# Kernel optimization log

Measured on AMD Instinct MI355X. Metric: run time of the kernel, lower is better.

Reference implementation:

```python
import jax, jax.numpy as jnp
import numpy as np

EPS = 1e-6
K = 20
B, N = 4, 4096
HID, CDIM = 128, 64


def vn_lin(W, x):
    # W: [Cout, Cin], x: [B, Cin, 3, ...] -> [B, Cout, 3, ...]
    return jnp.einsum('oc,bc...->bo...', W, x)


def vn_leaky(x, d, ns=0.0):
    # vector-neuron leaky ReLU: reflect the part of x anti-aligned with direction d
    dot = jnp.sum(x * d, axis=2, keepdims=True)
    dsq = jnp.sum(d * d, axis=2, keepdims=True)
    return ns * x + (1.0 - ns) * jnp.where(dot >= 0, x, x - (dot / (dsq + EPS)) * d)


def vn_max_pool(x, Wd):
    # pool over the LAST axis, picking per-(b,c) the vector maximizing <x, d>
    d = vn_lin(Wd, x)
    dot = jnp.sum(x * d, axis=2, keepdims=True)            # [B,C,1,...,L]
    idx = jnp.broadcast_to(jnp.argmax(dot, axis=-1), x.shape[:-1])
    return jnp.take_along_axis(x, idx[..., None], axis=-1)[..., 0]


def graph_feature_cross(pts, k):
    # pts: [B, N, 3] -> [B, 3ch, 3vec, N, k] with channels (nbr-x, x, cross(nbr,x))
    sq = jnp.sum(pts * pts, axis=-1)
    inner = jnp.einsum('bnd,bmd->bnm', pts, pts)
    neg_dist = 2.0 * inner - sq[:, :, None] - sq[:, None, :]
    _, idx = jax.lax.top_k(neg_dist, k)                     # [B, N, k]
    nbr = jax.vmap(lambda p, i: p[i])(pts, idx)             # [B, N, k, 3]
    x = jnp.broadcast_to(pts[:, :, None, :], nbr.shape)
    cross = jnp.cross(nbr, x, axis=-1)
    feat = jnp.stack([nbr - x, x, cross], axis=3)           # [B, N, k, 3ch, 3vec]
    return jnp.transpose(feat, (0, 3, 4, 1, 2))


def resblock(x, a0, f0, a1, f1, sc):
    net = vn_lin(f0, vn_leaky(x, vn_lin(a0, x)))
    dx = vn_lin(f1, vn_leaky(net, vn_lin(a1, net)))
    return vn_lin(sc, x) + dx


def _init(key, shape, fan_in):
    return jax.random.normal(key, shape, jnp.float32) / np.sqrt(fan_in)


def setup_inputs():
    key = jax.random.key(0)
    ks = jax.random.split(key, 14)
    return {
        'pc': jax.random.normal(ks[0], (B, N, 3), jnp.float32),
        'conv_Wf': _init(ks[1], (64, 3), 3),
        'conv_Wd': _init(ks[2], (64, 3), 3),
        'pool_pos_Wd': _init(ks[3], (64, 64), 64),
        'fc_pos_W': _init(ks[4], (2 * HID, 64), 64),
        'blk_a0': _init(ks[5], (5, 2 * HID, 2 * HID), 2 * HID),
        'blk_f0': _init(ks[6], (5, HID, 2 * HID), 2 * HID),
        'blk_a1': _init(ks[7], (5, HID, HID), HID),
        'blk_f1': _init(ks[8], (5, HID, HID), HID),
        'blk_sc': _init(ks[9], (5, HID, 2 * HID), 2 * HID),
        'pool_Wd': _init(ks[10], (5, HID, HID), HID),
        'actc_Wd': _init(ks[11], (HID, HID), HID),
        'fcc_W': _init(ks[12], (CDIM, HID), HID),
    }


def reference(pc, conv_Wf, conv_Wd, pool_pos_Wd, fc_pos_W, blk_a0, blk_f0, blk_a1, blk_f1, blk_sc, pool_Wd, actc_Wd, fcc_W):
    b = pc.shape[0]
    feat = graph_feature_cross(pc, K)                         # [B,3,3,N,k]
    net = vn_leaky(vn_lin(conv_Wf, feat), vn_lin(conv_Wd, feat))  # [B,64,3,N,k]
    net = vn_max_pool(net, pool_pos_Wd)                       # [B,64,3,N] (pool over k)
    net = vn_lin(fc_pos_W, net)                               # [B,256,3,N]
    for i in range(5):
        net = resblock(net, blk_a0[i], blk_f0[i], blk_a1[i], blk_f1[i], blk_sc[i])  # [B,128,3,N]
        if i < 4:
            pooled = vn_max_pool(net, pool_Wd[i])             # [B,128,3] (pool over N)
            net = jnp.concatenate([net, jnp.broadcast_to(pooled[..., None], net.shape)], axis=1)
    net = vn_max_pool(net, pool_Wd[4])                        # [B,128,3]
    c = vn_lin(fcc_W, vn_leaky(net, vn_lin(actc_Wd, net)))    # [B,64,3]
    return c.reshape(b, -1)                                   # [B,192]
```

## Files before the change

### kernel.cpp

```cpp
#include <hip/hip_runtime.h>
#include <hip/hip_bf16.h>
#include <math.h>

#define NPTS 4096
#define NB 4
#define KNN 20
#define NCOLS (3*NPTS)
#define NEG_INF (-__builtin_huge_valf())
#define DNEG_INF (-__builtin_huge_val())

typedef _Float16 f16x8 __attribute__((ext_vector_type(8)));
typedef float f32x4 __attribute__((ext_vector_type(4)));

#define WOFF_FC 0
#define WOFF_A0 16384
#define WOFF_F0 344064
#define WOFF_A1 507904
#define WOFF_F1 589824
#define WOFF_SC 671744
#define WOFF_PW 835584
#define WTOT    917504

__global__ __launch_bounds__(512) void knn_kernel(const float* __restrict__ pc,
                                                  int* __restrict__ idx) {
  __shared__ float pts[NPTS*3];
  __shared__ double msv[2][8];
  __shared__ int    msn[2][8];
  int b = blockIdx.x >> 10;
  int rowblk = blockIdx.x & 1023;
  const float* pb = pc + (size_t)b*NPTS*3;
  for (int i = threadIdx.x; i < NPTS*3; i += 512) pts[i] = pb[i];
  __syncthreads();
  int wave = threadIdx.x >> 6;
  int lane = threadIdx.x & 63;
  int row  = wave >> 1;
  int half = wave & 1;
  int l128 = half*64 + lane;
  int n = rowblk*4 + row;
  double pn0 = pts[n*3+0], pn1 = pts[n*3+1], pn2 = pts[n*3+2];
  double sqn = pn0*pn0 + pn1*pn1 + pn2*pn2;
  double nd[32];
#pragma unroll
  for (int j = 0; j < 32; ++j) {
    int m = j*128 + l128;
    double q0 = pts[m*3+0], q1 = pts[m*3+1], q2 = pts[m*3+2];
    double inner = pn0*q0 + pn1*q1 + pn2*q2;
    double sqm = q0*q0 + q1*q1 + q2*q2;
    nd[j] = 2.0*inner - sqn - sqm;
  }
  double gm[2]; int gj[2];
#pragma unroll
  for (int g = 0; g < 2; ++g) {
    double v = nd[g*16]; int jb = g*16;
#pragma unroll
    for (int jj = 1; jj < 16; ++jj) {
      int j = g*16 + jj;
      bool take = nd[j] > v;
      v = take ? nd[j] : v;
      jb = take ? j : jb;
    }
    gm[g] = v; gj[g] = jb;
  }
  int* orow = idx + ((size_t)b*NPTS + n)*KNN;
  for (int t = 0; t < KNN; ++t) {
    double bv = gm[0]; int bj = gj[0];
    if (gm[1] > bv) { bv = gm[1]; bj = gj[1]; }
    int bm = bj*128 + l128;
#pragma unroll
    for (int s = 1; s < 64; s <<= 1) {
      double ov = __shfl_xor(bv, s, 64);
      int om = __shfl_xor(bm, s, 64);
      bool take = (ov > bv) || (ov == bv && om < bm);
      bv = take ? ov : bv;
      bm = take ? om : bm;
    }
    if (lane == 0) { msv[t&1][wave] = bv; msn[t&1][wave] = bm; }
    __syncthreads();
    {
      double pv = msv[t&1][wave^1]; int pm = msn[t&1][wave^1];
      bool take = (pv > bv) || (pv == bv && pm < bm);
      bv = take ? pv : bv;
      bm = take ? pm : bm;
    }
    if (half == 0 && lane == 0) orow[t] = bm;
    if (t < KNN-1) {
      int vic_l128 = bm & 127;
      int jw = bm >> 7;
      int vic_half = vic_l128 >> 6;
      if (vic_half == half) {
        bool iswl = (l128 == vic_l128);
        int gw = jw >> 4;
#define REBUILD(G) { \
  _Pragma("unroll") \
  for (int jj = 0; jj < 16; ++jj) { \
    int j = (G)*16 + jj; \
    if (iswl && j == jw) nd[j] = DNEG_INF; \
  } \
  double v = nd[(G)*16]; int jb = (G)*16; \
  _Pragma("unroll") \
  for (int jj = 1; jj < 16; ++jj) { \
    int j = (G)*16 + jj; \
    bool take = nd[j] > v; \
    v = take ? nd[j] : v; \
    jb = take ? j : jb; \
  } \
  gm[G] = v; gj[G] = jb; \
}
        if (gw == 0) REBUILD(0)
        else         REBUILD(1)
#undef REBUILD
      }
    }
  }
}

#define ECH 5
__global__ __launch_bounds__(128) void edgeconv_kernel(
    const float* __restrict__ pc, const int* __restrict__ knnidx,
    const float* __restrict__ Wf, const float* __restrict__ Wd,
    const float* __restrict__ Wp, float* __restrict__ outp) {
  __shared__ float xls[2*ECH*3*64];
  int wave = threadIdx.x >> 6, lane = threadIdx.x & 63;
  int pid0 = blockIdx.x * 2;
  int b = pid0 >> 12;
  int n = (pid0 & (NPTS-1)) + wave;
  const float* pb = pc + (size_t)b*NPTS*3;
  int c = lane;
  float wrow[64];
#pragma unroll
  for (int j = 0; j < 64; ++j) wrow[j] = Wp[c*64 + j];
  float wf0 = Wf[c*3+0], wf1 = Wf[c*3+1], wf2 = Wf[c*3+2];
  float wd0 = Wd[c*3+0], wd1 = Wd[c*3+1], wd2 = Wd[c*3+2];
  float f9[9];
#pragma unroll
  for (int i = 0; i < 9; ++i) f9[i] = 0.0f;
  if (lane < KNN) {
    int j = knnidx[((size_t)b*NPTS + n)*KNN + lane];
    float q0 = pb[j*3+0], q1 = pb[j*3+1], q2 = pb[j*3+2];
    float x0 = pb[n*3+0], x1 = pb[n*3+1], x2 = pb[n*3+2];
    f9[0] = q0-x0; f9[1] = q1-x1; f9[2] = q2-x2;
    f9[3] = x0;    f9[4] = x1;    f9[5] = x2;
    f9[6] = q1*x2 - q2*x1;
    f9[7] = q2*x0 - q0*x2;
    f9[8] = q0*x1 - q1*x0;
  }
  float* xw = &xls[wave*ECH*3*64];
  double bdot = DNEG_INF;
  float bx0 = 0.f, bx1 = 0.f, bx2 = 0.f;
  for (int k0 = 0; k0 < KNN; k0 += ECH) {
    for (int kc = 0; kc < ECH; ++kc) {
      int kk = k0 + kc;
      float fch[9];
#pragma unroll
      for (int i = 0; i < 9; ++i) fch[i] = __shfl(f9[i], kk, 64);
      float fv[3], dv[3];
#pragma unroll
      for (int v = 0; v < 3; ++v) {
        fv[v] = wf0*fch[v] + wf1*fch[3+v] + wf2*fch[6+v];
        dv[v] = wd0*fch[v] + wd1*fch[3+v] + wd2*fch[6+v];
      }
      float dot = fv[0]*dv[0] + fv[1]*dv[1] + fv[2]*dv[2];
      if (dot < 0.0f) {
        float dsq = dv[0]*dv[0] + dv[1]*dv[1] + dv[2]*dv[2];
        float s = dot / (dsq + 1e-6f);
        fv[0] -= s*dv[0]; fv[1] -= s*dv[1]; fv[2] -= s*dv[2];
      }
      xw[(0*ECH+kc)*64 + c] = fv[0];
      xw[(1*ECH+kc)*64 + c] = fv[1];
      xw[(2*ECH+kc)*64 + c] = fv[2];
    }
    for (int kc = 0; kc < ECH; ++kc) {
      float a0 = 0.f, a1 = 0.f, a2 = 0.f;
#pragma unroll
      for (int j = 0; j < 64; j += 4) {
        float4 v0 = *(const float4*)&xw[(0*ECH+kc)*64 + j];
        float4 v1 = *(const float4*)&xw[(1*ECH+kc)*64 + j];
        float4 v2 = *(const float4*)&xw[(2*ECH+kc)*64 + j];
        a0 += wrow[j]*v0.x + wrow[j+1]*v0.y + wrow[j+2]*v0.z + wrow[j+3]*v0.w;
        a1 += wrow[j]*v1.x + wrow[j+1]*v1.y + wrow[j+2]*v1.z + wrow[j+3]*v1.w;
        a2 += wrow[j]*v2.x + wrow[j+1]*v2.y + wrow[j+2]*v2.z + wrow[j+3]*v2.w;
      }
      float xc0 = xw[(0*ECH+kc)*64 + c];
      float xc1 = xw[(1*ECH+kc)*64 + c];
      float xc2 = xw[(2*ECH+kc)*64 + c];
      double dd = (double)xc0*a0 + (double)xc1*a1 + (double)xc2*a2;
      bool take = dd > bdot;
      bdot = take ? dd : bdot;
      bx0 = take ? xc0 : bx0;
      bx1 = take ? xc1 : bx1;
      bx2 = take ? xc2 : bx2;
    }
  }
  outp[((size_t)b*NCOLS + 0*NPTS + n)*64 + c] = bx0;
  outp[((size_t)b*NCOLS + 1*NPTS + n)*64 + c] = bx1;
  outp[((size_t)b*NCOLS + 2*NPTS + n)*64 + c] = bx2;
}

__global__ __launch_bounds__(256) void wsplit_kernel(
    const float* __restrict__ fc, const float* __restrict__ a0,
    const float* __restrict__ f0, const float* __restrict__ a1,
    const float* __restrict__ f1, const float* __restrict__ sc,
    const float* __restrict__ pw, _Float16* __restrict__ outp) {
  int i = blockIdx.x*256 + threadIdx.x;
  const float* src; int off;
  if      (i < WOFF_A0) { src = fc; off = WOFF_FC; }
  else if (i < WOFF_F0) { src = a0; off = WOFF_A0; }
  else if (i < WOFF_A1) { src = f0; off = WOFF_F0; }
  else if (i < WOFF_F1) { src = a1; off = WOFF_A1; }
  else if (i < WOFF_SC) { src = f1; off = WOFF_F1; }
  else if (i < WOFF_PW) { src = sc; off = WOFF_SC; }
  else                  { src = pw; off = WOFF_PW; }
  float w = src[i - off];
  _Float16 h = (_Float16)w;
  outp[i] = h;
  outp[i + WTOT] = (_Float16)(w - (float)h);
}

__global__ __launch_bounds__(256) void bias_kernel(
    const float* __restrict__ W, const float* __restrict__ pooled,
    float* __restrict__ bias, int Cout, int Wstride) {
  int id = blockIdx.x*256 + threadIdx.x;
  int co = id % Cout; int t = id / Cout;
  int v = t % 3; int b = t / 3;
  double acc = 0.0;
  const float* wr = W + (size_t)co*Wstride + 128;
  const float* pp = pooled + (size_t)b*384 + v;
#pragma unroll 4
  for (int c = 0; c < 128; ++c)
    acc += (double)wr[c] * (double)pp[c*3];
  bias[id] = (float)acc;
}

#define LDP 40
__global__ __launch_bounds__(256) void gemm_mfma(
    const _Float16* __restrict__ Wh, const _Float16* __restrict__ Wl,
    const float* __restrict__ X, const float* __restrict__ Z,
    const float* __restrict__ bias, float* __restrict__ Y,
    int Cin, int Wstride, int ldX, int ldY, int ldZ, int addZ, int Cbias) {
  __shared__ __align__(16) _Float16 Ah[64*LDP];
  __shared__ __align__(16) _Float16 Al[64*LDP];
  __shared__ __align__(16) _Float16 Bh[128*LDP];
  __shared__ __align__(16) _Float16 Bl[128*LDP];
  int b = blockIdx.z;
  int sp0 = blockIdx.x * 64;
  int co0 = blockIdx.y * 128;
  const float* Xb = X + ((size_t)b*NCOLS + sp0) * ldX;
  int t = threadIdx.x;
  int arow = t >> 2, akoff = (t & 3) * 8;
  int brow = t >> 1, bkoff = (t & 1) * 16;
  int wid = t >> 6, lane = t & 63;
  int wr = (wid >> 1) * 32, wc = (wid & 1) * 64;
  int lrow = lane & 15, lk = (lane >> 4) * 8;
  f32x4 acc[2][4];
#pragma unroll
  for (int f = 0; f < 2; ++f)
#pragma unroll
    for (int g = 0; g < 4; ++g)
#pragma unroll
      for (int r = 0; r < 4; ++r) acc[f][g][r] = 0.0f;

  for (int k0 = 0; k0 < Cin; k0 += 32) {
    const float* xs = Xb + (size_t)arow*ldX + k0 + akoff;
    float xv[8];
    *(float4*)&xv[0] = *(const float4*)&xs[0];
    *(float4*)&xv[4] = *(const float4*)&xs[4];
    _Float16 xh[8], xl[8];
#pragma unroll
    for (int j = 0; j < 8; ++j) {
      _Float16 h = (_Float16)xv[j];
      xh[j] = h; xl[j] = (_Float16)(xv[j] - (float)h);
    }
    *(f16x8*)&Ah[arow*LDP + akoff] = *(f16x8*)&xh[0];
    *(f16x8*)&Al[arow*LDP + akoff] = *(f16x8*)&xl[0];
    const _Float16* whs = Wh + (size_t)(co0 + brow)*Wstride + k0 + bkoff;
    const _Float16* wls = Wl + (size_t)(co0 + brow)*Wstride + k0 + bkoff;
    *(f16x8*)&Bh[brow*LDP + bkoff]     = *(const f16x8*)&whs[0];
    *(f16x8*)&Bh[brow*LDP + bkoff + 8] = *(const f16x8*)&whs[8];
    *(f16x8*)&Bl[brow*LDP + bkoff]     = *(const f16x8*)&wls[0];
    *(f16x8*)&Bl[brow*LDP + bkoff + 8] = *(const f16x8*)&wls[8];
    __syncthreads();
    f16x8 ah[2], al[2], bh[4], bl[4];
#pragma unroll
    for (int f = 0; f < 2; ++f) {
      ah[f] = *(f16x8*)&Ah[(wr + f*16 + lrow)*LDP + lk];
      al[f] = *(f16x8*)&Al[(wr + f*16 + lrow)*LDP + lk];
    }
#pragma unroll
    for (int g = 0; g < 4; ++g) {
      bh[g] = *(f16x8*)&Bh[(wc + g*16 + lrow)*LDP + lk];
      bl[g] = *(f16x8*)&Bl[(wc + g*16 + lrow)*LDP + lk];
    }
#pragma unroll
    for (int f = 0; f < 2; ++f)
#pragma unroll
      for (int g = 0; g < 4; ++g) {
        acc[f][g] = __builtin_amdgcn_mfma_f32_16x16x32_f16(ah[f], bh[g], acc[f][g], 0, 0, 0);
        acc[f][g] = __builtin_amdgcn_mfma_f32_16x16x32_f16(ah[f], bl[g], acc[f][g], 0, 0, 0);
        acc[f][g] = __builtin_amdgcn_mfma_f32_16x16x32_f16(al[f], bh[g], acc[f][g], 0, 0, 0);
      }
    __syncthreads();
  }
  int lr0 = (lane >> 4) * 4, lc = lane & 15;
  float badd[4] = {0.f, 0.f, 0.f, 0.f};
  if (bias) {
    int v = sp0 >> 12;
    const float* brow2 = bias + ((size_t)b*3 + v)*Cbias;
#pragma unroll
    for (int g = 0; g < 4; ++g) badd[g] = brow2[co0 + wc + g*16 + lc];
  }
#pragma unroll
  for (int f = 0; f < 2; ++f)
#pragma unroll
    for (int g = 0; g < 4; ++g)
#pragma unroll
      for (int r = 0; r < 4; ++r) {
        int sp = sp0 + wr + f*16 + lr0 + r;
        int co = co0 + wc + g*16 + lc;
        float val = acc[f][g][r] + badd[g];
        if (addZ) val += Z[((size_t)b*NCOLS + sp)*ldZ + co];
        Y[((size_t)b*NCOLS + sp)*ldY + co] = val;
      }
}

__global__ __launch_bounds__(256) void leaky_kernel(
    const float* __restrict__ X, float* __restrict__ D,
    const float* __restrict__ pooled,
    int cmask, int cshift, int ld) {
  long id = (long)blockIdx.x*256 + threadIdx.x;
  int c = (int)(id & cmask);
  long r = id >> cshift;
  int n = (int)(r & (NPTS-1));
  int b = (int)(r >> 12);
  size_t base = ((size_t)b*NCOLS + n)*ld + c;
  size_t vs = (size_t)NPTS*ld;
  float x0, x1, x2;
  if (pooled != nullptr && c >= 128) {
    const float* pp = pooled + (size_t)b*384 + (c - 128)*3;
    x0 = pp[0]; x1 = pp[1]; x2 = pp[2];
  } else {
    x0 = X[base]; x1 = X[base+vs]; x2 = X[base+2*vs];
  }
  float d0 = D[base], d1 = D[base+vs], d2 = D[base+2*vs];
  float dot = x0*d0 + x1*d1 + x2*d2;
  float u0 = x0, u1 = x1, u2 = x2;
  if (dot < 0.0f) {
    float dsq = d0*d0 + d1*d1 + d2*d2;
    float s = dot / (dsq + 1e-6f);
    u0 = x0 - s*d0; u1 = x1 - s*d1; u2 = x2 - s*d2;
  }
  D[base] = u0; D[base+vs] = u1; D[base+2*vs] = u2;
}

__global__ __launch_bounds__(256) void pool1_kernel(
    const float* __restrict__ Net, const float* __restrict__ Dm,
    double* __restrict__ pv, int* __restrict__ pn, int ldN, int ldD) {
  __shared__ double sv[256];
  __shared__ int sn[256];
  int b = blockIdx.y;
  int n0 = blockIdx.x * 256;
  int c = threadIdx.x & 127;
  int half = threadIdx.x >> 7;
  double bv = DNEG_INF; int bn = 0x7fffffff;
  for (int i = 0; i < 128; ++i) {
    int n = n0 + 2*i + half;
    size_t r0 = ((size_t)b*NCOLS + n);
    double dot =
        (double)Net[(r0)*ldN + c]              * (double)Dm[(r0)*ldD + c]
      + (double)Net[(r0 + NPTS)*ldN + c]       * (double)Dm[(r0 + NPTS)*ldD + c]
      + (double)Net[(r0 + 2*NPTS)*ldN + c]     * (double)Dm[(r0 + 2*NPTS)*ldD + c];
    if (dot > bv) { bv = dot; bn = n; }
  }
  sv[threadIdx.x] = bv; sn[threadIdx.x] = bn;
  __syncthreads();
  if (half == 0) {
    double v1 = sv[threadIdx.x + 128]; int n1 = sn[threadIdx.x + 128];
    if (v1 > bv || (v1 == bv && n1 < bn)) { bv = v1; bn = n1; }
    pv[((size_t)b*16 + blockIdx.x)*128 + c] = bv;
    pn[((size_t)b*16 + blockIdx.x)*128 + c] = bn;
  }
}

__global__ __launch_bounds__(128) void pool2_kernel(
    const double* __restrict__ pv, const int* __restrict__ pn,
    const float* __restrict__ Net, float* __restrict__ pooled, int ldN) {
  int b = blockIdx.x, c = threadIdx.x;
  double bv = DNEG_INF; int bn = 0x7fffffff;
  for (int ch = 0; ch < 16; ++ch) {
    double v = pv[((size_t)b*16 + ch)*128 + c];
    int nn = pn[((size_t)b*16 + ch)*128 + c];
    if (v > bv || (v == bv && nn < bn)) { bv = v; bn = nn; }
  }
#pragma unroll
  for (int v = 0; v < 3; ++v)
    pooled[(size_t)b*384 + c*3 + v] = Net[((size_t)b*NCOLS + v*NPTS + bn)*ldN + c];
}

__global__ __launch_bounds__(128) void head_kernel(
    const float* __restrict__ pooled, const float* __restrict__ Wa,
    const float* __restrict__ Wc, float* __restrict__ out) {
  __shared__ float xp[128*3], up[128*3];
  int b = blockIdx.x, c = threadIdx.x;
#pragma unroll
  for (int v = 0; v < 3; ++v) xp[c*3+v] = pooled[(size_t)b*384 + c*3 + v];
  __syncthreads();
  float a0 = 0.f, a1 = 0.f, a2 = 0.f;
  for (int j = 0; j < 128; ++j) {
    float w = Wa[c*128+j];
    a0 += w*xp[j*3+0]; a1 += w*xp[j*3+1]; a2 += w*xp[j*3+2];
  }
  float x0 = xp[c*3+0], x1 = xp[c*3+1], x2 = xp[c*3+2];
  float dot = x0*a0 + x1*a1 + x2*a2;
  float u0 = x0, u1 = x1, u2 = x2;
  if (dot < 0.0f) {
    float dsq = a0*a0 + a1*a1 + a2*a2;
    float s = dot / (dsq + 1e-6f);
    u0 = x0 - s*a0; u1 = x1 - s*a1; u2 = x2 - s*a2;
  }
  up[c*3+0] = u0; up[c*3+1] = u1; up[c*3+2] = u2;
  __syncthreads();
  if (c < 64) {
    float o0 = 0.f, o1 = 0.f, o2 = 0.f;
    for (int j = 0; j < 128; ++j) {
      float w = Wc[c*128+j];
      o0 += w*up[j*3+0]; o1 += w*up[j*3+1]; o2 += w*up[j*3+2];
    }
    out[(size_t)b*192 + c*3 + 0] = o0;
    out[(size_t)b*192 + c*3 + 1] = o1;
    out[(size_t)b*192 + c*3 + 2] = o2;
  }
}

extern "C" void kernel_launch(void* const* d_in, const int* in_sizes, int n_in,
                              void* d_out, int out_size, void* d_ws, size_t ws_size,
                              hipStream_t stream) {
  const float* pc    = (const float*)d_in[0];
  const float* cWf   = (const float*)d_in[1];
  const float* cWd   = (const float*)d_in[2];
  const float* pposW = (const float*)d_in[3];
  const float* fcW   = (const float*)d_in[4];
  const float* ba0   = (const float*)d_in[5];
  const float* bf0   = (const float*)d_in[6];
  const float* ba1   = (const float*)d_in[7];
  const float* bf1   = (const float*)d_in[8];
  const float* bscW  = (const float*)d_in[9];
  const float* pWd   = (const float*)d_in[10];
  const float* aWd   = (const float*)d_in[11];
  const float* fccW  = (const float*)d_in[12];
  float* out = (float*)d_out;
  char* ws = (char*)d_ws;
  const size_t MB = 1u << 20;
  const size_t KB = 1u << 10;
  int*      idxb   = (int*)(ws);
  float*    X1     = (float*)(ws + 2*MB);
  float*    X2     = (float*)(ws + 52*MB);
  float*    conv   = (float*)(ws + 52*MB);
  float*    T      = (float*)(ws + 102*MB);
  float*    T2     = T;
  float*    DX     = (float*)(ws + 126*MB);
  float*    Hn     = (float*)(ws + 152*MB);
  float*    pooled = (float*)(ws + 178*MB);
  double*   pv     = (double*)(ws + 178*MB + 64*KB);
  int*      pn     = (int*)(ws + 178*MB + 128*KB);
  float*    biasA  = (float*)(ws + 178*MB + 256*KB);
  float*    biasS  = (float*)(ws + 178*MB + 320*KB);
  _Float16* Wsp    = (_Float16*)(ws + 179*MB);
  _Float16* WspLo  = Wsp + WTOT;

  wsplit_kernel<<<WTOT/256, 256, 0, stream>>>(fcW, ba0, bf0, ba1, bf1, bscW, pWd, Wsp);
  knn_kernel<<<NB*NPTS/4, 512, 0, stream>>>(pc, idxb);
  edgeconv_kernel<<<NB*NPTS/2, 128, 0, stream>>>(pc, idxb, cWf, cWd, pposW, conv);
  gemm_mfma<<<dim3(192, 2, NB), 256, 0, stream>>>(Wsp + WOFF_FC, WspLo + WOFF_FC,
      conv, nullptr, nullptr, X1, 64, 64, 64, 256, 0, 0, 0);

  float* Xin = X1; float* Xout = X2;
  for (int i = 0; i < 5; ++i) {
    const _Float16* a0h = Wsp   + WOFF_A0 + (size_t)i*65536;
    const _Float16* a0l = WspLo + WOFF_A0 + (size_t)i*65536;
    const _Float16* f0h = Wsp   + WOFF_F0 + (size_t)i*32768;
    const _Float16* f0l = WspLo + WOFF_F0 + (size_t)i*32768;
    const _Float16* a1h = Wsp   + WOFF_A1 + (size_t)i*16384;
    const _Float16* a1l = WspLo + WOFF_A1 + (size_t)i*16384;
    const _Float16* f1h = Wsp   + WOFF_F1 + (size_t)i*16384;
    const _Float16* f1l = WspLo + WOFF_F1 + (size_t)i*16384;
    const _Float16* sch = Wsp   + WOFF_SC + (size_t)i*32768;
    const _Float16* scl = WspLo + WOFF_SC + (size_t)i*32768;
    const _Float16* pwh = Wsp   + WOFF_PW + (size_t)i*16384;
    const _Float16* pwl = WspLo + WOFF_PW + (size_t)i*16384;
    int KA = (i == 0) ? 256 : 128;
    const float* bA = (i == 0) ? nullptr : biasA;
    const float* bS = (i == 0) ? nullptr : biasS;
    const float* lp = (i == 0) ? nullptr : pooled;
    if (i > 0) {
      bias_kernel<<<NB*3*256/256,256,0,stream>>>(ba0 + (size_t)i*65536, pooled, biasA, 256, 256);
      bias_kernel<<<NB*3*128/256,256,0,stream>>>(bscW + (size_t)i*32768, pooled, biasS, 128, 256);
    }
    gemm_mfma<<<dim3(192,2,NB),256,0,stream>>>(a0h, a0l, Xin, nullptr, bA, T,
        KA, 256, 256, 256, 0, 0, 256);
    leaky_kernel<<<NB*NPTS*256/256,256,0,stream>>>(Xin, T, lp, 255, 8, 256);
    gemm_mfma<<<dim3(192,1,NB),256,0,stream>>>(f0h, f0l, T, nullptr, nullptr, Hn,
        256, 256, 256, 128, 0, 0, 0);
    gemm_mfma<<<dim3(192,1,NB),256,0,stream>>>(a1h, a1l, Hn, nullptr, nullptr, T2,
        128, 128, 128, 128, 0, 0, 0);
    leaky_kernel<<<NB*NPTS*128/256,256,0,stream>>>(Hn, T2, nullptr, 127, 7, 128);
    gemm_mfma<<<dim3(192,1,NB),256,0,stream>>>(f1h, f1l, T2, nullptr, nullptr, DX,
        128, 128, 128, 128, 0, 0, 0);
    gemm_mfma<<<dim3(192,1,NB),256,0,stream>>>(sch, scl, Xin, DX, bS, Xout,
        KA, 256, 256, 256, 128, 1, 128);
    gemm_mfma<<<dim3(192,1,NB),256,0,stream>>>(pwh, pwl, Xout, nullptr, nullptr, Hn,
        128, 128, 256, 128, 0, 0, 0);
    pool1_kernel<<<dim3(16,NB),256,0,stream>>>(Xout, Hn, pv, pn, 256, 128);
    pool2_kernel<<<NB,128,0,stream>>>(pv, pn, Xout, pooled, 256);
    if (i < 4) { float* tmp = Xin; Xin = Xout; Xout = tmp; }
  }
  head_kernel<<<NB,128,0,stream>>>(pooled, aWd, fccW, out);
}
```

Measured before the change: 1.597 ms.

## Fuse VN leaky ReLU into direction GEMM computing all three vector components per block

Replaces the separate direction GEMM plus leaky_kernel pass with a templated gemm_leaky kernel. Each block accumulates the direction for all three vector components (v loop) in registers, then applies the vector-neuron leaky ReLU in the epilogue and writes the result directly. This removes a full write and re-read of the direction tensor and one kernel launch per use. In exchange it needs three times the accumulator registers per thread and uses smaller row tiles (FM=1 or 2), which may lower occupancy and MFMA efficiency.

```diff
diff --git a/kernel.cpp b/kernel.cpp
--- a/kernel.cpp
+++ b/kernel.cpp
@@ -10,6 +10,7 @@
 #define DNEG_INF (-__builtin_huge_val())
 
 typedef _Float16 f16x8 __attribute__((ext_vector_type(8)));
+typedef _Float16 f16x4 __attribute__((ext_vector_type(4)));
 typedef float f32x4 __attribute__((ext_vector_type(4)));
 
 #define WOFF_FC 0
@@ -322,33 +323,128 @@
       }
 }
 
-__global__ __launch_bounds__(256) void leaky_kernel(
-    const float* __restrict__ X, float* __restrict__ D,
-    const float* __restrict__ pooled,
-    int cmask, int cshift, int ld) {
-  long id = (long)blockIdx.x*256 + threadIdx.x;
-  int c = (int)(id & cmask);
-  long r = id >> cshift;
-  int n = (int)(r & (NPTS-1));
-  int b = (int)(r >> 12);
-  size_t base = ((size_t)b*NCOLS + n)*ld + c;
-  size_t vs = (size_t)NPTS*ld;
-  float x0, x1, x2;
-  if (pooled != nullptr && c >= 128) {
-    const float* pp = pooled + (size_t)b*384 + (c - 128)*3;
-    x0 = pp[0]; x1 = pp[1]; x2 = pp[2];
-  } else {
-    x0 = X[base]; x1 = X[base+vs]; x2 = X[base+2*vs];
-  }
-  float d0 = D[base], d1 = D[base+vs], d2 = D[base+2*vs];
-  float dot = x0*d0 + x1*d1 + x2*d2;
-  float u0 = x0, u1 = x1, u2 = x2;
-  if (dot < 0.0f) {
-    float dsq = d0*d0 + d1*d1 + d2*d2;
-    float s = dot / (dsq + 1e-6f);
-    u0 = x0 - s*d0; u1 = x1 - s*d1; u2 = x2 - s*d2;
-  }
-  D[base] = u0; D[base+vs] = u1; D[base+2*vs] = u2;
+template<int FM>
+__global__ __launch_bounds__(256) void gemm_leaky(
+    const _Float16* __restrict__ Wh, const _Float16* __restrict__ Wl,
+    const float* __restrict__ X, const float* __restrict__ pooled,
+    const float* __restrict__ bias, float* __restrict__ Y,
+    int Cin, int Wstride, int ldX, int ldY, int Cbias) {
+  constexpr int BM = FM*32;
+  __shared__ __align__(16) _Float16 Ah[BM*LDP];
+  __shared__ __align__(16) _Float16 Al[BM*LDP];
+  __shared__ __align__(16) _Float16 Bh[128*LDP];
+  __shared__ __align__(16) _Float16 Bl[128*LDP];
+  int b = blockIdx.z;
+  int n0 = blockIdx.x * BM;
+  int co0 = blockIdx.y * 128;
+  int t = threadIdx.x;
+  constexpr int APT = BM/8;
+  constexpr int TPR = 32/APT;
+  int arow = t / TPR, akoff = (t % TPR) * APT;
+  int brow = t >> 1, bkoff = (t & 1) * 16;
+  int wid = t >> 6, lane = t & 63;
+  int wr = (wid >> 1) * (BM/2), wc = (wid & 1) * 64;
+  int lrow = lane & 15, lk = (lane >> 4) * 8;
+  f32x4 acc[3][FM][4];
+#pragma unroll
+  for (int v = 0; v < 3; ++v)
+#pragma unroll
+    for (int f = 0; f < FM; ++f)
+#pragma unroll
+      for (int g = 0; g < 4; ++g)
+#pragma unroll
+        for (int r = 0; r < 4; ++r) acc[v][f][g][r] = 0.0f;
+
+  for (int v = 0; v < 3; ++v) {
+    const float* Xb = X + ((size_t)b*NCOLS + (size_t)v*NPTS + n0) * ldX;
+    for (int k0 = 0; k0 < Cin; k0 += 32) {
+      const float* xs = Xb + (size_t)arow*ldX + k0 + akoff;
+      float xv[APT];
+#pragma unroll
+      for (int j = 0; j < APT; j += 4)
+        *(float4*)&xv[j] = *(const float4*)&xs[j];
+      _Float16 xh[APT], xl[APT];
+#pragma unroll
+      for (int j = 0; j < APT; ++j) {
+        _Float16 h = (_Float16)xv[j];
+        xh[j] = h; xl[j] = (_Float16)(xv[j] - (float)h);
+      }
+      if (APT == 8) {
+        *(f16x8*)&Ah[arow*LDP + akoff] = *(f16x8*)&xh[0];
+        *(f16x8*)&Al[arow*LDP + akoff] = *(f16x8*)&xl[0];
+      } else {
+        *(f16x4*)&Ah[arow*LDP + akoff] = *(f16x4*)&xh[0];
+        *(f16x4*)&Al[arow*LDP + akoff] = *(f16x4*)&xl[0];
+      }
+      const _Float16* whs = Wh + (size_t)(co0 + brow)*Wstride + k0 + bkoff;
+      const _Float16* wls = Wl + (size_t)(co0 + brow)*Wstride + k0 + bkoff;
+      *(f16x8*)&Bh[brow*LDP + bkoff]     = *(const f16x8*)&whs[0];
+      *(f16x8*)&Bh[brow*LDP + bkoff + 8] = *(const f16x8*)&whs[8];
+      *(f16x8*)&Bl[brow*LDP + bkoff]     = *(const f16x8*)&wls[0];
+      *(f16x8*)&Bl[brow*LDP + bkoff + 8] = *(const f16x8*)&wls[8];
+      __syncthreads();
+      f16x8 ah[FM], al[FM], bh[4], bl[4];
+#pragma unroll
+      for (int f = 0; f < FM; ++f) {
+        ah[f] = *(f16x8*)&Ah[(wr + f*16 + lrow)*LDP + lk];
+        al[f] = *(f16x8*)&Al[(wr + f*16 + lrow)*LDP + lk];
+      }
+#pragma unroll
+      for (int g = 0; g < 4; ++g) {
+        bh[g] = *(f16x8*)&Bh[(wc + g*16 + lrow)*LDP + lk];
+        bl[g] = *(f16x8*)&Bl[(wc + g*16 + lrow)*LDP + lk];
+      }
+#pragma unroll
+      for (int f = 0; f < FM; ++f)
+#pragma unroll
+        for (int g = 0; g < 4; ++g) {
+          acc[v][f][g] = __builtin_amdgcn_mfma_f32_16x16x32_f16(ah[f], bh[g], acc[v][f][g], 0, 0, 0);
+          acc[v][f][g] = __builtin_amdgcn_mfma_f32_16x16x32_f16(ah[f], bl[g], acc[v][f][g], 0, 0, 0);
+          acc[v][f][g] = __builtin_amdgcn_mfma_f32_16x16x32_f16(al[f], bh[g], acc[v][f][g], 0, 0, 0);
+        }
+      __syncthreads();
+    }
+  }
+  int lr0 = (lane >> 4) * 4, lc = lane & 15;
+  float badd[3][4];
+#pragma unroll
+  for (int v = 0; v < 3; ++v)
+#pragma unroll
+    for (int g = 0; g < 4; ++g) {
+      badd[v][g] = bias ? bias[((size_t)b*3 + v)*Cbias + co0 + wc + g*16 + lc] : 0.0f;
+    }
+  bool xfromX = (pooled == nullptr) || (co0 < 128);
+#pragma unroll
+  for (int f = 0; f < FM; ++f)
+#pragma unroll
+    for (int g = 0; g < 4; ++g)
+#pragma unroll
+      for (int r = 0; r < 4; ++r) {
+        int n = n0 + wr + f*16 + lr0 + r;
+        int co = co0 + wc + g*16 + lc;
+        float x0, x1, x2;
+        if (xfromX) {
+          x0 = X[((size_t)b*NCOLS + 0*NPTS + n)*ldX + co];
+          x1 = X[((size_t)b*NCOLS + 1*NPTS + n)*ldX + co];
+          x2 = X[((size_t)b*NCOLS + 2*NPTS + n)*ldX + co];
+        } else {
+          const float* pp = pooled + (size_t)b*384 + (co - 128)*3;
+          x0 = pp[0]; x1 = pp[1]; x2 = pp[2];
+        }
+        float d0 = acc[0][f][g][r] + badd[0][g];
+        float d1 = acc[1][f][g][r] + badd[1][g];
+        float d2 = acc[2][f][g][r] + badd[2][g];
+        float dot = x0*d0 + x1*d1 + x2*d2;
+        float u0 = x0, u1 = x1, u2 = x2;
+        if (dot < 0.0f) {
+          float dsq = d0*d0 + d1*d1 + d2*d2;
+          float s = dot / (dsq + 1e-6f);
+          u0 = x0 - s*d0; u1 = x1 - s*d1; u2 = x2 - s*d2;
+        }
+        Y[((size_t)b*NCOLS + 0*NPTS + n)*ldY + co] = u0;
+        Y[((size_t)b*NCOLS + 1*NPTS + n)*ldY + co] = u1;
+        Y[((size_t)b*NCOLS + 2*NPTS + n)*ldY + co] = u2;
+      }
 }
 
 __global__ __launch_bounds__(256) void pool1_kernel(
@@ -494,14 +590,12 @@
       bias_kernel<<<NB*3*256/256,256,0,stream>>>(ba0 + (size_t)i*65536, pooled, biasA, 256, 256);
       bias_kernel<<<NB*3*128/256,256,0,stream>>>(bscW + (size_t)i*32768, pooled, biasS, 128, 256);
     }
-    gemm_mfma<<<dim3(192,2,NB),256,0,stream>>>(a0h, a0l, Xin, nullptr, bA, T,
-        KA, 256, 256, 256, 0, 0, 256);
-    leaky_kernel<<<NB*NPTS*256/256,256,0,stream>>>(Xin, T, lp, 255, 8, 256);
+    gemm_leaky<2><<<dim3(NPTS/64, 2, NB), 256, 0, stream>>>(a0h, a0l, Xin, lp, bA, T,
+        KA, 256, 256, 256, 256);
     gemm_mfma<<<dim3(192,1,NB),256,0,stream>>>(f0h, f0l, T, nullptr, nullptr, Hn,
         256, 256, 256, 128, 0, 0, 0);
-    gemm_mfma<<<dim3(192,1,NB),256,0,stream>>>(a1h, a1l, Hn, nullptr, nullptr, T2,
-        128, 128, 128, 128, 0, 0, 0);
-    leaky_kernel<<<NB*NPTS*128/256,256,0,stream>>>(Hn, T2, nullptr, 127, 7, 128);
+    gemm_leaky<1><<<dim3(NPTS/32, 1, NB), 256, 0, stream>>>(a1h, a1l, Hn, nullptr, nullptr, T2,
+        128, 128, 128, 128, 0);
     gemm_mfma<<<dim3(192,1,NB),256,0,stream>>>(f1h, f1l, T2, nullptr, nullptr, DX,
         128, 128, 128, 128, 0, 0, 0);
     gemm_mfma<<<dim3(192,1,NB),256,0,stream>>>(sch, scl, Xin, DX, bS, Xout,
```

Result: faster. 1.549 ms (-3.0%).
